# Performance work log

Hardware: AMD Instinct MI355X
Metric: run time of the kernel (lower is better)

Reference implementation:

```python
import jax, jax.numpy as jnp
import numpy as np

N_HEADS = 16
D_EMBED = 1024
D_CROSS = 768
D_HEAD = D_EMBED // N_HEADS
B, S = 4, 2048


def setup_inputs() -> dict:
    key = jax.random.key(0)
    ks = jax.random.split(key, 10)
    sq = lambda k, shp, fan: jax.random.normal(k, shp, jnp.float32) / np.sqrt(fan)
    return {
        "x": jax.random.normal(ks[0], (B, S, D_EMBED), jnp.float32),
        "y": jax.random.normal(ks[1], (B, S, D_CROSS), jnp.float32),
        "Wq": sq(ks[2], (D_EMBED, D_EMBED), D_EMBED),
        "bq": jnp.zeros((D_EMBED,), jnp.float32),
        "Wk": sq(ks[3], (D_CROSS, D_EMBED), D_CROSS),
        "bk": jnp.zeros((D_EMBED,), jnp.float32),
        "Wv": sq(ks[4], (D_CROSS, D_EMBED), D_CROSS),
        "bv": jnp.zeros((D_EMBED,), jnp.float32),
        "Wo": sq(ks[5], (D_EMBED, D_EMBED), D_EMBED),
        "bo": jnp.zeros((D_EMBED,), jnp.float32),
    }


def reference(x, y, Wq, bq, Wk, bk, Wv, bv, Wo, bo):
    b, s, _ = y.shape
    q = x @ Wq + bq  # [b, s, d_embed]
    k = y @ Wk + bk
    v = y @ Wv + bv
    # [b, h, s, d_head]
    q = q.reshape(b, s, N_HEADS, D_HEAD).transpose(0, 2, 1, 3)
    k = k.reshape(b, s, N_HEADS, D_HEAD).transpose(0, 2, 1, 3)
    v = v.reshape(b, s, N_HEADS, D_HEAD).transpose(0, 2, 1, 3)
    scale = 1.0 / np.sqrt(D_HEAD).astype(np.float32)
    scores = jnp.einsum("bhqd,bhkd->bhqk", q, k) * scale
    weights = jax.nn.softmax(scores, axis=-1)
    out = jnp.einsum("bhqk,bhkd->bhqd", weights, v)
    out = out.transpose(0, 2, 1, 3).reshape(x.shape)
    return out @ Wo + bo
```

## Files before the change

kernel.cpp:

```cpp
#include <hip/hip_runtime.h>

#define NHEADS 16
#define DEMBED 1024
#define DCROSS 768
#define DHEAD  64
#define BATCH  4
#define SLEN   2048
#define MROWS  (BATCH * SLEN)

using bf16   = __bf16;
using bf16x8 = __attribute__((ext_vector_type(8))) __bf16;
using bf16x4 = __attribute__((ext_vector_type(4))) __bf16;
using f32x4  = __attribute__((ext_vector_type(4))) float;

__device__ __forceinline__ f32x4 mfma_bf16(bf16x8 a, bf16x8 b, f32x4 c) {
    return __builtin_amdgcn_mfma_f32_16x16x32_bf16(a, b, c, 0, 0, 0);
}

__device__ __forceinline__ void gl2lds16(const void* g, void* l) {
    __builtin_amdgcn_global_load_lds(
        (const __attribute__((address_space(1))) void*)g,
        (__attribute__((address_space(3))) void*)l, 16, 0, 0);
}

__global__ void cvt_f32_bf16(const float* __restrict__ in, bf16* __restrict__ out, int n4) {
    int i = blockIdx.x * blockDim.x + threadIdx.x;
    if (i >= n4) return;
    float4 v = ((const float4*)in)[i];
    bf16x4 o = { (bf16)v.x, (bf16)v.y, (bf16)v.z, (bf16)v.w };
    ((bf16x4*)out)[i] = o;
}

__global__ void transpose_cvt(const float* __restrict__ W, bf16* __restrict__ Wt, int K, int N) {
    __shared__ float tile[32][33];
    int n0 = blockIdx.x * 32, k0 = blockIdx.y * 32;
    int tx = threadIdx.x, ty = threadIdx.y;
#pragma unroll
    for (int i = 0; i < 32; i += 8)
        tile[ty + i][tx] = W[(size_t)(k0 + ty + i) * N + n0 + tx];
    __syncthreads();
#pragma unroll
    for (int i = 0; i < 32; i += 8)
        Wt[(size_t)(n0 + ty + i) * K + k0 + tx] = (bf16)tile[tx][ty + i];
}

template <bool F32OUT>
__global__ __launch_bounds__(256, 3) void gemm_bt(const bf16* __restrict__ A,
                                                  const bf16* __restrict__ Bt,
                                                  const float* __restrict__ bias,
                                                  void* __restrict__ Cout,
                                                  int M, int N, int K, float alpha) {
    __shared__ bf16 As[128 * 32];
    __shared__ bf16 Bs[128 * 32];
    const int tid  = threadIdx.x;
    const int wave = tid >> 6, lane = tid & 63;
    const int quad = lane >> 4, l15 = lane & 15;
    const int m0 = blockIdx.x * 128, n0 = blockIdx.y * 128;
    const int wr = wave >> 1, wc = wave & 1;

    const int trow = tid >> 2;
    const int tcol = ((tid & 3) ^ ((tid >> 3) & 3)) * 8;
    char* ldsA0 = (char*)As + wave * 1024;
    char* ldsB0 = (char*)Bs + wave * 1024;
    const bf16* gA0 = A + (size_t)(m0 + trow) * K + tcol;
    const bf16* gA1 = A + (size_t)(m0 + 64 + trow) * K + tcol;
    const bf16* gB0 = Bt + (size_t)(n0 + trow) * K + tcol;
    const bf16* gB1 = Bt + (size_t)(n0 + 64 + trow) * K + tcol;

    const int sw = (l15 >> 1) & 3;

    f32x4 acc[4][4] = {};

    for (int kt = 0; kt < K; kt += 32) {
        __syncthreads();
        gl2lds16(gA0 + kt, ldsA0);
        gl2lds16(gA1 + kt, ldsA0 + 4096);
        gl2lds16(gB0 + kt, ldsB0);
        gl2lds16(gB1 + kt, ldsB0 + 4096);
        __syncthreads();

        bf16x8 af[4], bfr[4];
#pragma unroll
        for (int i = 0; i < 4; i++)
            af[i] = *(const bf16x8*)((const char*)As +
                     (wr * 64 + i * 16 + l15) * 64 + ((quad ^ sw) * 16));
#pragma unroll
        for (int i = 0; i < 4; i++)
            bfr[i] = *(const bf16x8*)((const char*)Bs +
                     (wc * 64 + i * 16 + l15) * 64 + ((quad ^ sw) * 16));
#pragma unroll
        for (int fr = 0; fr < 4; fr++)
#pragma unroll
            for (int fc = 0; fc < 4; fc++)
                acc[fr][fc] = mfma_bf16(af[fr], bfr[fc], acc[fr][fc]);
    }

#pragma unroll
    for (int fr = 0; fr < 4; fr++) {
        int row = m0 + wr * 64 + fr * 16 + quad * 4;
#pragma unroll
        for (int fc = 0; fc < 4; fc++) {
            int col = n0 + wc * 64 + fc * 16 + l15;
            float bv = bias[col];
#pragma unroll
            for (int r = 0; r < 4; r++) {
                float v = (acc[fr][fc][r] + bv) * alpha;
                if (F32OUT)
                    ((float*)Cout)[(size_t)(row + r) * N + col] = v;
                else
                    ((bf16*)Cout)[(size_t)(row + r) * N + col] = (bf16)v;
            }
        }
    }
}

__global__ __launch_bounds__(256, 3) void gemm_vt(const bf16* __restrict__ Wvt,
                                                  const bf16* __restrict__ Yb,
                                                  const float* __restrict__ bias,
                                                  bf16* __restrict__ Vt) {
    const int K = DCROSS;
    __shared__ bf16 As[128 * 32];
    __shared__ bf16 Bs[128 * 32];
    const int tid  = threadIdx.x;
    const int wave = tid >> 6, lane = tid & 63;
    const int quad = lane >> 4, l15 = lane & 15;
    const int m0 = blockIdx.x * 128;
    const int n0 = blockIdx.y * 128;
    const int wr = wave >> 1, wc = wave & 1;

    const int trow = tid >> 2;
    const int tcol = ((tid & 3) ^ ((tid >> 3) & 3)) * 8;
    char* ldsA0 = (char*)As + wave * 1024;
    char* ldsB0 = (char*)Bs + wave * 1024;
    const bf16* gA0 = Wvt + (size_t)(m0 + trow) * K + tcol;
    const bf16* gA1 = Wvt + (size_t)(m0 + 64 + trow) * K + tcol;
    const bf16* gB0 = Yb + (size_t)(n0 + trow) * K + tcol;
    const bf16* gB1 = Yb + (size_t)(n0 + 64 + trow) * K + tcol;

    const int sw = (l15 >> 1) & 3;

    f32x4 acc[4][4] = {};

    for (int kt = 0; kt < K; kt += 32) {
        __syncthreads();
        gl2lds16(gA0 + kt, ldsA0);
        gl2lds16(gA1 + kt, ldsA0 + 4096);
        gl2lds16(gB0 + kt, ldsB0);
        gl2lds16(gB1 + kt, ldsB0 + 4096);
        __syncthreads();

        bf16x8 af[4], bfr[4];
#pragma unroll
        for (int i = 0; i < 4; i++)
            af[i] = *(const bf16x8*)((const char*)As +
                     (wr * 64 + i * 16 + l15) * 64 + ((quad ^ sw) * 16));
#pragma unroll
        for (int i = 0; i < 4; i++)
            bfr[i] = *(const bf16x8*)((const char*)Bs +
                     (wc * 64 + i * 16 + l15) * 64 + ((quad ^ sw) * 16));
#pragma unroll
        for (int fr = 0; fr < 4; fr++)
#pragma unroll
            for (int fc = 0; fc < 4; fc++)
                acc[fr][fc] = mfma_bf16(af[fr], bfr[fc], acc[fr][fc]);
    }

    const int b = n0 >> 11;
    const size_t bbase = (size_t)b * DEMBED * SLEN;
#pragma unroll
    for (int fr = 0; fr < 4; fr++) {
        int row = m0 + wr * 64 + fr * 16 + quad * 4;
#pragma unroll
        for (int fc = 0; fc < 4; fc++) {
            int col = n0 + wc * 64 + fc * 16 + l15;
            int s = col & (SLEN - 1);
#pragma unroll
            for (int r = 0; r < 4; r++) {
                float v = acc[fr][fc][r] + bias[row + r];
                Vt[bbase + (size_t)(row + r) * SLEN + s] = (bf16)v;
            }
        }
    }
}

__global__ __launch_bounds__(256, 4) void attn(const bf16* __restrict__ Q,
                                               const bf16* __restrict__ K,
                                               const bf16* __restrict__ Vt,
                                               bf16* __restrict__ O) {
    __shared__ bf16 KsA[64 * 64];
    __shared__ bf16 VsA[64 * 64];
    __shared__ bf16 PsA[4 * 32 * 72];

    const int tid  = threadIdx.x;
    const int wave = tid >> 6, lane = tid & 63;
    const int quad = lane >> 4, l15 = lane & 15;
    const int bh = blockIdx.y, b = bh >> 4, h = bh & 15;
    const size_t rowbase = (size_t)b * SLEN;
    const int qb = blockIdx.x * 128 + wave * 32;
    const int hc = h * DHEAD;

    bf16x8 qf[2][2];
#pragma unroll
    for (int rg = 0; rg < 2; rg++)
#pragma unroll
        for (int kg = 0; kg < 2; kg++)
            qf[rg][kg] = *(const bf16x8*)(Q + (rowbase + qb + rg * 16 + l15) * DEMBED
                                          + hc + kg * 32 + quad * 8);

    f32x4 o[2][4] = {};
    f32x4 lsv[2] = {};

    const bf16* Kbase = K + rowbase * DEMBED + hc;
    const bf16* Vbase = Vt + (size_t)bh * DHEAD * SLEN;

    const int xcol = (((tid & 7) ^ ((tid >> 3) & 7)) * 8);
    const bf16* gK = Kbase + (size_t)(tid >> 3) * DEMBED + xcol;
    const bf16* gV = Vbase + (size_t)(tid >> 3) * SLEN + xcol;
    char* ldsK = (char*)KsA + wave * 1024;
    char* ldsV = (char*)VsA + wave * 1024;
    bf16* Pw = PsA + wave * (32 * 72);

    for (int kb = 0; kb < SLEN; kb += 64) {
        __syncthreads();
        gl2lds16(gK + (size_t)kb * DEMBED, ldsK);
        gl2lds16(gK + (size_t)(kb + 32) * DEMBED, ldsK + 32 * 128);
        gl2lds16(gV + kb, ldsV);
        gl2lds16(gV + 32 * SLEN + kb, ldsV + 32 * 128);
        __syncthreads();

        f32x4 s[2][4] = {};
#pragma unroll
        for (int cg = 0; cg < 4; cg++)
#pragma unroll
            for (int kg = 0; kg < 2; kg++) {
                bf16x8 kf = *(const bf16x8*)((const char*)KsA +
                            (cg * 16 + l15) * 128 + (((kg * 4 + quad) ^ (l15 & 7)) * 16));
#pragma unroll
                for (int rg = 0; rg < 2; rg++)
                    s[rg][cg] = mfma_bf16(kf, qf[rg][kg], s[rg][cg]);
            }

#pragma unroll
        for (int rg = 0; rg < 2; rg++)
#pragma unroll
            for (int cg = 0; cg < 4; cg++) {
                f32x4 p;
                p[0] = __builtin_amdgcn_exp2f(s[rg][cg][0]);
                p[1] = __builtin_amdgcn_exp2f(s[rg][cg][1]);
                p[2] = __builtin_amdgcn_exp2f(s[rg][cg][2]);
                p[3] = __builtin_amdgcn_exp2f(s[rg][cg][3]);
                lsv[rg] += p;
                bf16x4 pb = { (bf16)p[0], (bf16)p[1], (bf16)p[2], (bf16)p[3] };
                *(bf16x4*)(Pw + (rg * 16 + l15) * 72 + cg * 16 + quad * 4) = pb;
            }

#pragma unroll
        for (int dg = 0; dg < 4; dg++)
#pragma unroll
            for (int kg = 0; kg < 2; kg++) {
                bf16x8 vf = *(const bf16x8*)((const char*)VsA +
                            (dg * 16 + l15) * 128 + (((kg * 4 + quad) ^ (l15 & 7)) * 16));
#pragma unroll
                for (int rg = 0; rg < 2; rg++)
                    o[rg][dg] = mfma_bf16(
                        *(const bf16x8*)(Pw + (rg * 16 + l15) * 72 + kg * 32 + quad * 8),
                        vf, o[rg][dg]);
            }
    }

    float inv[2];
#pragma unroll
    for (int rg = 0; rg < 2; rg++) {
        float rs = lsv[rg][0] + lsv[rg][1] + lsv[rg][2] + lsv[rg][3];
        rs += __shfl_xor(rs, 16);
        rs += __shfl_xor(rs, 32);
        inv[rg] = 1.0f / rs;
    }
#pragma unroll
    for (int rg = 0; rg < 2; rg++)
#pragma unroll
        for (int r = 0; r < 4; r++) {
            float iv = __shfl(inv[rg], quad * 4 + r);
#pragma unroll
            for (int dg = 0; dg < 4; dg++)
                O[(rowbase + qb + rg * 16 + quad * 4 + r) * DEMBED + hc + dg * 16 + l15] =
                    (bf16)(o[rg][dg][r] * iv);
        }
}

extern "C" void kernel_launch(void* const* d_in, const int* in_sizes, int n_in,
                              void* d_out, int out_size, void* d_ws, size_t ws_size,
                              hipStream_t stream) {
    const float* x  = (const float*)d_in[0];
    const float* y  = (const float*)d_in[1];
    const float* Wq = (const float*)d_in[2];
    const float* bq = (const float*)d_in[3];
    const float* Wk = (const float*)d_in[4];
    const float* bk = (const float*)d_in[5];
    const float* Wv = (const float*)d_in[6];
    const float* bv = (const float*)d_in[7];
    const float* Wo = (const float*)d_in[8];
    const float* bo = (const float*)d_in[9];
    float* out = (float*)d_out;

    char* ws = (char*)d_ws;
    size_t off = 0;
    auto alloc = [&](size_t bytes) {
        void* p = ws + off;
        off += (bytes + 255) & ~(size_t)255;
        return p;
    };
    bf16* xb  = (bf16*)alloc((size_t)MROWS * DEMBED * 2);
    bf16* yb  = (bf16*)alloc((size_t)MROWS * DCROSS * 2);
    bf16* Wqt = (bf16*)alloc((size_t)DEMBED * DEMBED * 2);
    bf16* Wkt = (bf16*)alloc((size_t)DEMBED * DCROSS * 2);
    bf16* Wvt = (bf16*)alloc((size_t)DEMBED * DCROSS * 2);
    bf16* Wot = (bf16*)alloc((size_t)DEMBED * DEMBED * 2);
    bf16* Qb  = (bf16*)alloc((size_t)MROWS * DEMBED * 2);
    bf16* Kb  = (bf16*)alloc((size_t)MROWS * DEMBED * 2);
    bf16* Vtb = (bf16*)alloc((size_t)MROWS * DEMBED * 2);
    bf16* Ab  = (bf16*)alloc((size_t)MROWS * DEMBED * 2);
    if (off > ws_size) return;

    {
        int n4 = MROWS * DEMBED / 4;
        cvt_f32_bf16<<<(n4 + 255) / 256, 256, 0, stream>>>(x, xb, n4);
    }
    {
        int n4 = MROWS * DCROSS / 4;
        cvt_f32_bf16<<<(n4 + 255) / 256, 256, 0, stream>>>(y, yb, n4);
    }
    transpose_cvt<<<dim3(DEMBED / 32, DEMBED / 32), dim3(32, 8), 0, stream>>>(Wq, Wqt, DEMBED, DEMBED);
    transpose_cvt<<<dim3(DEMBED / 32, DCROSS / 32), dim3(32, 8), 0, stream>>>(Wk, Wkt, DCROSS, DEMBED);
    transpose_cvt<<<dim3(DEMBED / 32, DCROSS / 32), dim3(32, 8), 0, stream>>>(Wv, Wvt, DCROSS, DEMBED);
    transpose_cvt<<<dim3(DEMBED / 32, DEMBED / 32), dim3(32, 8), 0, stream>>>(Wo, Wot, DEMBED, DEMBED);

    const float qscale = 0.125f * 1.4426950408889634f;
    dim3 gg(MROWS / 128, DEMBED / 128);
    gemm_bt<false><<<gg, 256, 0, stream>>>(xb, Wqt, bq, Qb, MROWS, DEMBED, DEMBED, qscale);
    gemm_bt<false><<<gg, 256, 0, stream>>>(yb, Wkt, bk, Kb, MROWS, DEMBED, DCROSS, 1.0f);
    gemm_vt<<<dim3(DEMBED / 128, MROWS / 128), 256, 0, stream>>>(Wvt, yb, bv, Vtb);

    attn<<<dim3(SLEN / 128, BATCH * NHEADS), 256, 0, stream>>>(Qb, Kb, Vtb, Ab);

    gemm_bt<true><<<gg, 256, 0, stream>>>(Ab, Wot, bo, out, MROWS, DEMBED, DEMBED, 1.0f);
}
```

Measured before the change: 308.2 us.

## Batch conversion, transpose and QKV GEMMs into single launches; retile output GEMM

Merges the two input conversions into one kernel and the four weight transposes into one 3D-grid launch. The Q, K and V^T projections become one 1536-block kernel that picks its operands from the block index. The output projection gets a dedicated 128x64-tile kernel with higher occupancy and more blocks. This cuts launch count and tail gaps between small kernels, and lets the three projections fill the device together. The cost is a branchy prologue and epilogue in the fused GEMM and smaller output-GEMM tiles with less operand reuse.

Measured after the change: 303.2 us. About the same (-1.6%).

```diff
diff --git a/kernel.cpp b/kernel.cpp
--- a/kernel.cpp
+++ b/kernel.cpp
@@ -23,17 +23,31 @@
         (__attribute__((address_space(3))) void*)l, 16, 0, 0);
 }
 
-__global__ void cvt_f32_bf16(const float* __restrict__ in, bf16* __restrict__ out, int n4) {
+__global__ void cvt_xy(const float* __restrict__ x, const float* __restrict__ y,
+                       bf16* __restrict__ xb, bf16* __restrict__ yb) {
+    const int n4x = MROWS * DEMBED / 4;
+    const int n4y = MROWS * DCROSS / 4;
     int i = blockIdx.x * blockDim.x + threadIdx.x;
-    if (i >= n4) return;
-    float4 v = ((const float4*)in)[i];
+    const float* src;
+    bf16* dst;
+    int j;
+    if (i < n4x) { src = x; dst = xb; j = i; }
+    else { j = i - n4x; if (j >= n4y) return; src = y; dst = yb; }
+    float4 v = ((const float4*)src)[j];
     bf16x4 o = { (bf16)v.x, (bf16)v.y, (bf16)v.z, (bf16)v.w };
-    ((bf16x4*)out)[i] = o;
-}
-
-__global__ void transpose_cvt(const float* __restrict__ W, bf16* __restrict__ Wt, int K, int N) {
+    ((bf16x4*)dst)[j] = o;
+}
+
+struct TrArgs { const float* src[4]; bf16* dst[4]; int K[4]; };
+__global__ void transpose_all(TrArgs a) {
     __shared__ float tile[32][33];
+    const int which = blockIdx.z;
+    const int K = a.K[which];
+    const int N = DEMBED;
     int n0 = blockIdx.x * 32, k0 = blockIdx.y * 32;
+    if (k0 >= K) return;
+    const float* W = a.src[which];
+    bf16* Wt = a.dst[which];
     int tx = threadIdx.x, ty = threadIdx.y;
 #pragma unroll
     for (int i = 0; i < 32; i += 8)
@@ -44,18 +58,30 @@
         Wt[(size_t)(n0 + ty + i) * K + k0 + tx] = (bf16)tile[tx][ty + i];
 }
 
-template <bool F32OUT>
-__global__ __launch_bounds__(256, 3) void gemm_bt(const bf16* __restrict__ A,
-                                                  const bf16* __restrict__ Bt,
-                                                  const float* __restrict__ bias,
-                                                  void* __restrict__ Cout,
-                                                  int M, int N, int K, float alpha) {
+struct QkvArgs {
+    const bf16 *xb, *yb, *Wqt, *Wkt, *Wvt;
+    const float *bq, *bk, *bv;
+    bf16 *Qb, *Kb, *Vt;
+    float qscale;
+};
+__global__ __launch_bounds__(256, 3) void gemm_qkv(QkvArgs a) {
     __shared__ bf16 As[128 * 32];
     __shared__ bf16 Bs[128 * 32];
+    const int id = blockIdx.x;
+    const int cls = id >> 9;
+    const bf16 *A, *Bt;
+    const float* bias;
+    int K, m0, n0;
+    if (cls == 0) { int t = id;        m0 = (t >> 3) * 128; n0 = (t & 7) * 128;
+                    A = a.xb;  Bt = a.Wqt; bias = a.bq; K = DEMBED; }
+    else if (cls == 1) { int t = id - 512;  m0 = (t >> 3) * 128; n0 = (t & 7) * 128;
+                    A = a.yb;  Bt = a.Wkt; bias = a.bk; K = DCROSS; }
+    else { int t = id - 1024; m0 = (t >> 6) * 128; n0 = (t & 63) * 128;
+                    A = a.Wvt; Bt = a.yb;  bias = a.bv; K = DCROSS; }
+
     const int tid  = threadIdx.x;
     const int wave = tid >> 6, lane = tid & 63;
     const int quad = lane >> 4, l15 = lane & 15;
-    const int m0 = blockIdx.x * 128, n0 = blockIdx.y * 128;
     const int wr = wave >> 1, wc = wave & 1;
 
     const int trow = tid >> 2;
@@ -95,90 +121,98 @@
                 acc[fr][fc] = mfma_bf16(af[fr], bfr[fc], acc[fr][fc]);
     }
 
-#pragma unroll
-    for (int fr = 0; fr < 4; fr++) {
-        int row = m0 + wr * 64 + fr * 16 + quad * 4;
-#pragma unroll
-        for (int fc = 0; fc < 4; fc++) {
-            int col = n0 + wc * 64 + fc * 16 + l15;
-            float bv = bias[col];
-#pragma unroll
-            for (int r = 0; r < 4; r++) {
-                float v = (acc[fr][fc][r] + bv) * alpha;
-                if (F32OUT)
-                    ((float*)Cout)[(size_t)(row + r) * N + col] = v;
-                else
-                    ((bf16*)Cout)[(size_t)(row + r) * N + col] = (bf16)v;
+    if (cls < 2) {
+        bf16* Cout = (cls == 0) ? a.Qb : a.Kb;
+        const float alpha = (cls == 0) ? a.qscale : 1.0f;
+#pragma unroll
+        for (int fr = 0; fr < 4; fr++) {
+            int row = m0 + wr * 64 + fr * 16 + quad * 4;
+#pragma unroll
+            for (int fc = 0; fc < 4; fc++) {
+                int col = n0 + wc * 64 + fc * 16 + l15;
+                float bv = bias[col];
+#pragma unroll
+                for (int r = 0; r < 4; r++)
+                    Cout[(size_t)(row + r) * DEMBED + col] =
+                        (bf16)((acc[fr][fc][r] + bv) * alpha);
             }
         }
-    }
-}
-
-__global__ __launch_bounds__(256, 3) void gemm_vt(const bf16* __restrict__ Wvt,
-                                                  const bf16* __restrict__ Yb,
-                                                  const float* __restrict__ bias,
-                                                  bf16* __restrict__ Vt) {
-    const int K = DCROSS;
+    } else {
+        const int b = n0 >> 11;
+        const size_t bbase = (size_t)b * DEMBED * SLEN;
+#pragma unroll
+        for (int fr = 0; fr < 4; fr++) {
+            int row = m0 + wr * 64 + fr * 16 + quad * 4;
+#pragma unroll
+            for (int fc = 0; fc < 4; fc++) {
+                int col = n0 + wc * 64 + fc * 16 + l15;
+                int s = col & (SLEN - 1);
+#pragma unroll
+                for (int r = 0; r < 4; r++)
+                    a.Vt[bbase + (size_t)(row + r) * SLEN + s] =
+                        (bf16)(acc[fr][fc][r] + bias[row + r]);
+            }
+        }
+    }
+}
+
+__global__ __launch_bounds__(256, 4) void gemm_o(const bf16* __restrict__ A,
+                                                 const bf16* __restrict__ Bt,
+                                                 const float* __restrict__ bias,
+                                                 float* __restrict__ Cout) {
+    const int K = DEMBED, N = DEMBED;
     __shared__ bf16 As[128 * 32];
-    __shared__ bf16 Bs[128 * 32];
+    __shared__ bf16 Bs[64 * 32];
     const int tid  = threadIdx.x;
     const int wave = tid >> 6, lane = tid & 63;
     const int quad = lane >> 4, l15 = lane & 15;
-    const int m0 = blockIdx.x * 128;
-    const int n0 = blockIdx.y * 128;
-    const int wr = wave >> 1, wc = wave & 1;
+    const int m0 = blockIdx.x * 128, n0 = blockIdx.y * 64;
 
     const int trow = tid >> 2;
     const int tcol = ((tid & 3) ^ ((tid >> 3) & 3)) * 8;
     char* ldsA0 = (char*)As + wave * 1024;
     char* ldsB0 = (char*)Bs + wave * 1024;
-    const bf16* gA0 = Wvt + (size_t)(m0 + trow) * K + tcol;
-    const bf16* gA1 = Wvt + (size_t)(m0 + 64 + trow) * K + tcol;
-    const bf16* gB0 = Yb + (size_t)(n0 + trow) * K + tcol;
-    const bf16* gB1 = Yb + (size_t)(n0 + 64 + trow) * K + tcol;
+    const bf16* gA0 = A + (size_t)(m0 + trow) * K + tcol;
+    const bf16* gA1 = A + (size_t)(m0 + 64 + trow) * K + tcol;
+    const bf16* gB0 = Bt + (size_t)(n0 + trow) * K + tcol;
 
     const int sw = (l15 >> 1) & 3;
 
-    f32x4 acc[4][4] = {};
+    f32x4 acc[2][4] = {};
 
     for (int kt = 0; kt < K; kt += 32) {
         __syncthreads();
         gl2lds16(gA0 + kt, ldsA0);
         gl2lds16(gA1 + kt, ldsA0 + 4096);
         gl2lds16(gB0 + kt, ldsB0);
-        gl2lds16(gB1 + kt, ldsB0 + 4096);
-        __syncthreads();
-
-        bf16x8 af[4], bfr[4];
-#pragma unroll
-        for (int i = 0; i < 4; i++)
+        __syncthreads();
+
+        bf16x8 af[2], bfr[4];
+#pragma unroll
+        for (int i = 0; i < 2; i++)
             af[i] = *(const bf16x8*)((const char*)As +
-                     (wr * 64 + i * 16 + l15) * 64 + ((quad ^ sw) * 16));
+                     (wave * 32 + i * 16 + l15) * 64 + ((quad ^ sw) * 16));
 #pragma unroll
         for (int i = 0; i < 4; i++)
             bfr[i] = *(const bf16x8*)((const char*)Bs +
-                     (wc * 64 + i * 16 + l15) * 64 + ((quad ^ sw) * 16));
-#pragma unroll
-        for (int fr = 0; fr < 4; fr++)
+                     (i * 16 + l15) * 64 + ((quad ^ sw) * 16));
+#pragma unroll
+        for (int fr = 0; fr < 2; fr++)
 #pragma unroll
             for (int fc = 0; fc < 4; fc++)
                 acc[fr][fc] = mfma_bf16(af[fr], bfr[fc], acc[fr][fc]);
     }
 
-    const int b = n0 >> 11;
-    const size_t bbase = (size_t)b * DEMBED * SLEN;
-#pragma unroll
-    for (int fr = 0; fr < 4; fr++) {
-        int row = m0 + wr * 64 + fr * 16 + quad * 4;
+#pragma unroll
+    for (int fr = 0; fr < 2; fr++) {
+        int row = m0 + wave * 32 + fr * 16 + quad * 4;
 #pragma unroll
         for (int fc = 0; fc < 4; fc++) {
-            int col = n0 + wc * 64 + fc * 16 + l15;
-            int s = col & (SLEN - 1);
-#pragma unroll
-            for (int r = 0; r < 4; r++) {
-                float v = acc[fr][fc][r] + bias[row + r];
-                Vt[bbase + (size_t)(row + r) * SLEN + s] = (bf16)v;
-            }
+            int col = n0 + fc * 16 + l15;
+            float bv = bias[col];
+#pragma unroll
+            for (int r = 0; r < 4; r++)
+                Cout[(size_t)(row + r) * N + col] = acc[fr][fc][r] + bv;
         }
     }
 }
@@ -323,25 +357,28 @@
     if (off > ws_size) return;
 
     {
-        int n4 = MROWS * DEMBED / 4;
-        cvt_f32_bf16<<<(n4 + 255) / 256, 256, 0, stream>>>(x, xb, n4);
+        int n4 = MROWS * DEMBED / 4 + MROWS * DCROSS / 4;
+        cvt_xy<<<(n4 + 255) / 256, 256, 0, stream>>>(x, y, xb, yb);
     }
     {
-        int n4 = MROWS * DCROSS / 4;
-        cvt_f32_bf16<<<(n4 + 255) / 256, 256, 0, stream>>>(y, yb, n4);
-    }
-    transpose_cvt<<<dim3(DEMBED / 32, DEMBED / 32), dim3(32, 8), 0, stream>>>(Wq, Wqt, DEMBED, DEMBED);
-    transpose_cvt<<<dim3(DEMBED / 32, DCROSS / 32), dim3(32, 8), 0, stream>>>(Wk, Wkt, DCROSS, DEMBED);
-    transpose_cvt<<<dim3(DEMBED / 32, DCROSS / 32), dim3(32, 8), 0, stream>>>(Wv, Wvt, DCROSS, DEMBED);
-    transpose_cvt<<<dim3(DEMBED / 32, DEMBED / 32), dim3(32, 8), 0, stream>>>(Wo, Wot, DEMBED, DEMBED);
-
-    const float qscale = 0.125f * 1.4426950408889634f;
-    dim3 gg(MROWS / 128, DEMBED / 128);
-    gemm_bt<false><<<gg, 256, 0, stream>>>(xb, Wqt, bq, Qb, MROWS, DEMBED, DEMBED, qscale);
-    gemm_bt<false><<<gg, 256, 0, stream>>>(yb, Wkt, bk, Kb, MROWS, DEMBED, DCROSS, 1.0f);
-    gemm_vt<<<dim3(DEMBED / 128, MROWS / 128), 256, 0, stream>>>(Wvt, yb, bv, Vtb);
+        TrArgs a;
+        a.src[0] = Wq;  a.dst[0] = Wqt; a.K[0] = DEMBED;
+        a.src[1] = Wk;  a.dst[1] = Wkt; a.K[1] = DCROSS;
+        a.src[2] = Wv;  a.dst[2] = Wvt; a.K[2] = DCROSS;
+        a.src[3] = Wo;  a.dst[3] = Wot; a.K[3] = DEMBED;
+        transpose_all<<<dim3(32, 32, 4), dim3(32, 8), 0, stream>>>(a);
+    }
+
+    {
+        QkvArgs a;
+        a.xb = xb; a.yb = yb; a.Wqt = Wqt; a.Wkt = Wkt; a.Wvt = Wvt;
+        a.bq = bq; a.bk = bk; a.bv = bv;
+        a.Qb = Qb; a.Kb = Kb; a.Vt = Vtb;
+        a.qscale = 0.125f * 1.4426950408889634f;
+        gemm_qkv<<<1536, 256, 0, stream>>>(a);
+    }
 
     attn<<<dim3(SLEN / 128, BATCH * NHEADS), 256, 0, stream>>>(Qb, Kb, Vtb, Ab);
 
-    gemm_bt<true><<<gg, 256, 0, stream>>>(Ab, Wot, bo, out, MROWS, DEMBED, DEMBED, 1.0f);
-}
+    gemm_o<<<dim3(MROWS / 128, DEMBED / 64), 256, 0, stream>>>(Ab, Wot, bo, out);
+}
```
